# Kernel tuning notes

Measured on AMD Instinct MI355X. Metric: run time of the kernel, lower is better.

The kernel has to match this reference:

```python
import jax, jax.numpy as jnp
import numpy as np

B = 64        # number of graphs
NPG = 4096    # nodes per graph (equal-size segments, batch ids sorted)
H = 256       # hidden_dim
C0, C1 = 256, 64  # num_clusters


def setup_inputs() -> dict:
    key = jax.random.key(0)
    ks = jax.random.split(key, 8)
    N = B * NPG
    x = jax.random.normal(ks[0], (N, H), dtype=jnp.float32)
    edge_index = jax.random.randint(ks[1], (2, N), 0, N, dtype=jnp.int64)  # unused by forward
    batch = jnp.repeat(jnp.arange(B, dtype=jnp.int64), NPG)  # sorted, equal-size segments
    s = 1.0 / np.sqrt(H)
    W0 = jax.random.uniform(ks[2], (H, C0), jnp.float32, -s, s)
    b0 = jax.random.uniform(ks[3], (C0,), jnp.float32, -s, s)
    W1 = jax.random.uniform(ks[4], (H, C1), jnp.float32, -s, s)
    b1 = jax.random.uniform(ks[5], (C1,), jnp.float32, -s, s)
    sf = 1.0 / np.sqrt(C1 * H)
    Wf = jax.random.uniform(ks[6], (C1 * H, H), jnp.float32, -sf, sf)
    bf = jax.random.uniform(ks[7], (H,), jnp.float32, -sf, sf)
    return {"x": x, "edge_index": edge_index, "batch": batch,
            "W0": W0, "b0": b0, "W1": W1, "b1": b1, "Wf": Wf, "bf": bf}


def reference(x, edge_index, batch, W0, b0, W1, b1, Wf, bf):
    # Level 0: softmax cluster assignment + per-graph segmented matmul A^T @ F.
    # batch ids are sorted with equal-size segments, so the per-graph Python
    # loop of the original collapses to a reshape + batched einsum.
    A0 = jax.nn.softmax(x @ W0 + b0, axis=-1)                      # [N, C0]
    f0 = jnp.einsum('bnc,bnh->bch',
                    A0.reshape(B, NPG, C0),
                    x.reshape(B, NPG, H)).reshape(B * C0, H)        # [B*C0, H]
    # Level 1: same pattern on pooled cluster features (C0 'nodes' per graph).
    A1 = jax.nn.softmax(f0 @ W1 + b1, axis=-1)                     # [B*C0, C1]
    f1 = jnp.einsum('bnc,bnh->bch',
                    A1.reshape(B, C0, C1),
                    f0.reshape(B, C0, H)).reshape(B, C1 * H)        # [B, C1*H]
    # Final pool: Linear -> ReLU (Dropout is identity in eval mode).
    return jax.nn.relu(f1 @ Wf + bf)                               # [B, H]
```

## Files before the change

### kernel.cpp

```cpp
#include <hip/hip_runtime.h>
#include <stdint.h>

#define NG   64
#define NPG  4096
#define HD   256
#define NC0  256
#define NC1  64
#define KSPLIT 2

typedef __attribute__((ext_vector_type(8))) short bfx8;
typedef __attribute__((ext_vector_type(4))) float fx4;

__device__ __forceinline__ unsigned short f2bf(float f) {
  union { float f; unsigned int u; } v; v.f = f;
  return (unsigned short)((v.u + 0x7FFFu + ((v.u >> 16) & 1u)) >> 16);
}
__device__ __forceinline__ unsigned int pack2(float a, float b) {
  return (unsigned int)f2bf(a) | ((unsigned int)f2bf(b) << 16);
}

#define ASYNC_COPY16(gptr, lptr) \
  __builtin_amdgcn_global_load_lds((const __attribute__((address_space(1))) unsigned int*)(gptr), \
                                   (__attribute__((address_space(3))) unsigned int*)(lptr), 16, 0, 0)

__global__ __launch_bounds__(256) void k_w0f(const float* __restrict__ W0,
                                             unsigned short* __restrict__ W0F) {
  int gid = blockIdx.x * 256 + threadIdx.x;
  int l15 = gid & 15;
  int q   = (gid >> 4) & 3;
  int ks  = (gid >> 6) & 1;
  int kc  = (gid >> 7) & 3;
  int cblk = gid >> 9;
  int c = cblk * 16 + l15;
  int kb = kc * 64 + ks * 32 + q * 8;
  unsigned int u[4];
  #pragma unroll
  for (int j = 0; j < 8; j += 2)
    u[j >> 1] = pack2(W0[(size_t)(kb + j) * 256 + c], W0[(size_t)(kb + j + 1) * 256 + c]);
  *(float4*)(W0F + (size_t)gid * 8) = *(float4*)u;
}

__global__ __launch_bounds__(512, 4) void k_assign0(
    const float* __restrict__ x, const unsigned short* __restrict__ W0F,
    const float* __restrict__ b0, unsigned short* __restrict__ A0T,
    unsigned short* __restrict__ xT, int g0) {
  __shared__ unsigned short lds_u[18432];
  __shared__ float red[512];

  int gl = blockIdx.x >> 5, nt = blockIdx.x & 31;
  int tid = threadIdx.x;
  int wave = tid >> 6, lane = tid & 63;
  int wm = wave >> 2, wn = wave & 3;
  int l15 = lane & 15, q = lane >> 4;

  fx4 acc[4][4];
  #pragma unroll
  for (int i = 0; i < 4; ++i)
    #pragma unroll
    for (int j = 0; j < 4; ++j) acc[i][j] = fx4{0.f, 0.f, 0.f, 0.f};

  const float* xbase = x + ((size_t)(g0 + gl) * NPG + (size_t)nt * 128) * HD;
  int snode = tid >> 2;
  int sseg  = (tid & 3) * 16;
  int sg0   = (tid & 3) * 2;
  int ssw   = (snode ^ (snode >> 4)) & 7;

  bfx8 bvc[4], bvn[4];
  #pragma unroll
  for (int ni = 0; ni < 4; ++ni)
    bvc[ni] = *(const bfx8*)(W0F + ((size_t)(((wn * 4 + ni) * 8 + 0) * 64 + lane)) * 8);

  {
    const float4* src = (const float4*)(xbase + (size_t)snode * HD + sseg);
    float4 v0 = src[0], v1 = src[1], v2 = src[2], v3 = src[3];
    float4 pv[2]; unsigned int* pu = (unsigned int*)pv;
    pu[0] = pack2(v0.x, v0.y); pu[1] = pack2(v0.z, v0.w);
    pu[2] = pack2(v1.x, v1.y); pu[3] = pack2(v1.z, v1.w);
    pu[4] = pack2(v2.x, v2.y); pu[5] = pack2(v2.z, v2.w);
    pu[6] = pack2(v3.x, v3.y); pu[7] = pack2(v3.z, v3.w);
    unsigned short* drow = &lds_u[snode << 6];
    *(float4*)(drow + (((sg0    ) ^ ssw) << 3)) = pv[0];
    *(float4*)(drow + (((sg0 + 1) ^ ssw) << 3)) = pv[1];
  }
  __syncthreads();

  #pragma unroll
  for (int kc = 0; kc < 4; ++kc) {
    const unsigned short* xb = &lds_u[(kc & 1) * 8192];
    float4 v0, v1, v2, v3;
    if (kc < 3) {
      const float4* src = (const float4*)(xbase + (size_t)snode * HD + (kc + 1) * 64 + sseg);
      v0 = src[0]; v1 = src[1]; v2 = src[2]; v3 = src[3];
    }
    #pragma unroll
    for (int ks = 0; ks < 2; ++ks) {
      int g8 = kc * 2 + ks;
      if (g8 < 7) {
        #pragma unroll
        for (int ni = 0; ni < 4; ++ni)
          bvn[ni] = *(const bfx8*)(W0F + ((size_t)(((wn * 4 + ni) * 8 + g8 + 1) * 64 + lane)) * 8);
      }
      bfx8 af[4];
      #pragma unroll
      for (int mi = 0; mi < 4; ++mi) {
        int row = wm * 64 + mi * 16 + l15;
        int slot = (ks * 4 + q) ^ ((row ^ (row >> 4)) & 7);
        af[mi] = *(const bfx8*)&xb[(row << 6) + (slot << 3)];
      }
      #pragma unroll
      for (int ni = 0; ni < 4; ++ni)
        #pragma unroll
        for (int mi = 0; mi < 4; ++mi)
          acc[mi][ni] = __builtin_amdgcn_mfma_f32_16x16x32_bf16(af[mi], bvc[ni], acc[mi][ni], 0, 0, 0);
      if (g8 < 7) {
        #pragma unroll
        for (int ni = 0; ni < 4; ++ni) bvc[ni] = bvn[ni];
      }
    }
    #pragma unroll
    for (int p2 = 0; p2 < 2; ++p2) {
      int hl = p2 * 32 + wave * 4 + (lane >> 4);
      int g = hl >> 3, off = hl & 7;
      int nb = (lane & 15) * 8;
      unsigned int u[4];
      #pragma unroll
      for (int j = 0; j < 8; j += 2) {
        int n0 = nb + j, n1 = n0 + 1;
        unsigned short a = xb[(n0 << 6) + ((g ^ ((n0 ^ (n0 >> 4)) & 7)) << 3) + off];
        unsigned short b = xb[(n1 << 6) + ((g ^ ((n1 ^ (n1 >> 4)) & 7)) << 3) + off];
        u[j >> 1] = (unsigned int)a | ((unsigned int)b << 16);
      }
      *(float4*)(xT + ((size_t)gl * HD + kc * 64 + hl) * NPG + (size_t)nt * 128 + nb) = *(float4*)u;
    }
    if (kc < 3) {
      float4 pv[2]; unsigned int* pu = (unsigned int*)pv;
      pu[0] = pack2(v0.x, v0.y); pu[1] = pack2(v0.z, v0.w);
      pu[2] = pack2(v1.x, v1.y); pu[3] = pack2(v1.z, v1.w);
      pu[4] = pack2(v2.x, v2.y); pu[5] = pack2(v2.z, v2.w);
      pu[6] = pack2(v3.x, v3.y); pu[7] = pack2(v3.z, v3.w);
      unsigned short* drow = &lds_u[(((kc & 1) ^ 1) * 8192) + (snode << 6)];
      *(float4*)(drow + (((sg0    ) ^ ssw) << 3)) = pv[0];
      *(float4*)(drow + (((sg0 + 1) ^ ssw) << 3)) = pv[1];
    }
    __syncthreads();
  }

  float bv4[4];
  #pragma unroll
  for (int ni = 0; ni < 4; ++ni) bv4[ni] = b0[wn * 64 + ni * 16 + l15];
  #pragma unroll
  for (int mi = 0; mi < 4; ++mi)
    #pragma unroll
    for (int ni = 0; ni < 4; ++ni)
      #pragma unroll
      for (int r = 0; r < 4; ++r) acc[mi][ni][r] += bv4[ni];

  float mrow[4][4];
  #pragma unroll
  for (int mi = 0; mi < 4; ++mi)
    #pragma unroll
    for (int r = 0; r < 4; ++r) {
      float m = fmaxf(fmaxf(acc[mi][0][r], acc[mi][1][r]), fmaxf(acc[mi][2][r], acc[mi][3][r]));
      #pragma unroll
      for (int off = 1; off < 16; off <<= 1) m = fmaxf(m, __shfl_xor(m, off));
      mrow[mi][r] = m;
    }
  if (l15 == 0) {
    #pragma unroll
    for (int mi = 0; mi < 4; ++mi)
      #pragma unroll
      for (int r = 0; r < 4; ++r)
        red[(wm * 64 + mi * 16 + q * 4 + r) * 4 + wn] = mrow[mi][r];
  }
  __syncthreads();
  #pragma unroll
  for (int mi = 0; mi < 4; ++mi)
    #pragma unroll
    for (int r = 0; r < 4; ++r) {
      float4 rv = *(const float4*)&red[(wm * 64 + mi * 16 + q * 4 + r) * 4];
      mrow[mi][r] = fmaxf(fmaxf(rv.x, rv.y), fmaxf(rv.z, rv.w));
    }
  __syncthreads();
  float srow[4][4];
  #pragma unroll
  for (int mi = 0; mi < 4; ++mi)
    #pragma unroll
    for (int r = 0; r < 4; ++r) {
      float s = 0.f;
      #pragma unroll
      for (int ni = 0; ni < 4; ++ni) {
        float e = __expf(acc[mi][ni][r] - mrow[mi][r]);
        acc[mi][ni][r] = e; s += e;
      }
      #pragma unroll
      for (int off = 1; off < 16; off <<= 1) s += __shfl_xor(s, off);
      srow[mi][r] = s;
    }
  if (l15 == 0) {
    #pragma unroll
    for (int mi = 0; mi < 4; ++mi)
      #pragma unroll
      for (int r = 0; r < 4; ++r)
        red[(wm * 64 + mi * 16 + q * 4 + r) * 4 + wn] = srow[mi][r];
  }
  __syncthreads();
  #pragma unroll
  for (int mi = 0; mi < 4; ++mi)
    #pragma unroll
    for (int r = 0; r < 4; ++r) {
      float4 rv = *(const float4*)&red[(wm * 64 + mi * 16 + q * 4 + r) * 4];
      float inv = 1.f / (rv.x + rv.y + rv.z + rv.w);
      #pragma unroll
      for (int ni = 0; ni < 4; ++ni) acc[mi][ni][r] *= inv;
    }
  __syncthreads();

  unsigned short* at = lds_u;
  unsigned short* A0Tg = A0T + (size_t)gl * NC0 * NPG + (size_t)nt * 128;
  #pragma unroll
  for (int p = 0; p < 2; ++p) {
    if ((wn >> 1) == p) {
      int cb = (wn & 1) * 64;
      #pragma unroll
      for (int mi = 0; mi < 4; ++mi) {
        int ncol = wm * 64 + mi * 16 + q * 4;
        #pragma unroll
        for (int ni = 0; ni < 4; ++ni) {
          int cl = cb + ni * 16 + l15;
          uint2 w;
          w.x = pack2(acc[mi][ni][0], acc[mi][ni][1]);
          w.y = pack2(acc[mi][ni][2], acc[mi][ni][3]);
          *(uint2*)(at + cl * 144 + ncol) = w;
        }
      }
    }
    __syncthreads();
    #pragma unroll
    for (int rp = 0; rp < 4; ++rp) {
      int row = rp * 32 + wave * 4 + (lane >> 4);
      int nb = (lane & 15) * 8;
      bfx8 vv = *(const bfx8*)(at + row * 144 + nb);
      *(bfx8*)(A0Tg + (size_t)(p * 128 + row) * NPG + nb) = vv;
    }
    __syncthreads();
  }
}

__global__ __launch_bounds__(256, 2) void k_pool0(
    const unsigned short* __restrict__ A0T, const unsigned short* __restrict__ xT,
    float* __restrict__ f0p, int g0) {
  __shared__ unsigned short a_s[128 * 64];
  __shared__ unsigned short b_s[128 * 64];
  int bid = blockIdx.x;
  int kidx = bid & 1;
  int nt = (bid >> 1) & 1;
  int mt = (bid >> 2) & 1;
  int gl = bid >> 3;

  int tid = threadIdx.x;
  int wave = tid >> 6, lane = tid & 63;
  int wm = wave >> 1, wnn = wave & 1;
  int l15 = lane & 15, q = lane >> 4;

  const int KPER = NPG / KSPLIT;
  const unsigned short* abase = A0T + ((size_t)gl * NC0 + (size_t)mt * 128) * NPG + (size_t)kidx * KPER;
  const unsigned short* bbase = xT  + ((size_t)gl * HD  + (size_t)nt * 128) * NPG + (size_t)kidx * KPER;

  fx4 acc[4][4];
  #pragma unroll
  for (int i = 0; i < 4; ++i)
    #pragma unroll
    for (int j = 0; j < 4; ++j) acc[i][j] = fx4{0.f, 0.f, 0.f, 0.f};

  int srow = lane >> 3;
  int sg   = (lane & 7) ^ srow;
  size_t soff = (size_t)srow * NPG + (size_t)sg * 8;

  for (int k0 = 0; k0 < KPER; k0 += 64) {
    #pragma unroll
    for (int i = 0; i < 4; ++i) {
      int r0 = wave * 32 + i * 8;
      ASYNC_COPY16(abase + (size_t)r0 * NPG + k0 + soff, &a_s[r0 * 64]);
      ASYNC_COPY16(bbase + (size_t)r0 * NPG + k0 + soff, &b_s[r0 * 64]);
    }
    __syncthreads();
    #pragma unroll
    for (int ks = 0; ks < 2; ++ks) {
      int gx = ((ks * 4 + q) ^ (l15 & 7)) << 3;
      bfx8 af[4], bf[4];
      #pragma unroll
      for (int mi = 0; mi < 4; ++mi)
        af[mi] = *(const bfx8*)&a_s[(wm * 64 + mi * 16 + l15) * 64 + gx];
      #pragma unroll
      for (int ni = 0; ni < 4; ++ni)
        bf[ni] = *(const bfx8*)&b_s[(wnn * 64 + ni * 16 + l15) * 64 + gx];
      #pragma unroll
      for (int ni = 0; ni < 4; ++ni)
        #pragma unroll
        for (int mi = 0; mi < 4; ++mi)
          acc[mi][ni] = __builtin_amdgcn_mfma_f32_16x16x32_bf16(af[mi], bf[ni], acc[mi][ni], 0, 0, 0);
    }
    __syncthreads();
  }

  float* dst = f0p + (size_t)kidx * NG * NC0 * HD
             + ((size_t)(g0 + gl) * NC0 + (size_t)mt * 128) * HD + (size_t)nt * 128;
  #pragma unroll
  for (int mi = 0; mi < 4; ++mi)
    #pragma unroll
    for (int ni = 0; ni < 4; ++ni) {
      int c = wm * 64 + mi * 16 + q * 4;
      int h = wnn * 64 + ni * 16 + l15;
      #pragma unroll
      for (int r = 0; r < 4; ++r)
        dst[(size_t)(c + r) * HD + h] = acc[mi][ni][r];
    }
}

__global__ __launch_bounds__(256) void k_f0sum(float* __restrict__ f0) {
  size_t i = ((size_t)blockIdx.x * 256 + threadIdx.x) * 4;
  float4 a = *(const float4*)(f0 + i);
  float4 b = *(const float4*)(f0 + (size_t)NG * NC0 * HD + i);
  a.x += b.x; a.y += b.y; a.z += b.z; a.w += b.w;
  *(float4*)(f0 + i) = a;
}

__global__ __launch_bounds__(256) void k_assign1(
    const float* __restrict__ f0, const float* __restrict__ W1,
    const float* __restrict__ b1, float* __restrict__ A1) {
  __shared__ float w1s[256 * 64];
  int tid = threadIdx.x;
  #pragma unroll
  for (int i = 0; i < 16; ++i) {
    int off = i * 1024 + tid * 4;
    *(float4*)(w1s + off) = *(const float4*)(W1 + off);
  }
  __syncthreads();
  int lane = tid & 63;
  int rbase = blockIdx.x * 32 + (tid >> 6) * 8;
  float bias = b1[lane];
  for (int rr = 0; rr < 8; ++rr) {
    int row = rbase + rr;
    const float* fr = f0 + (size_t)row * 256;
    float acc = bias;
    for (int k = 0; k < 256; k += 4) {
      float4 fv = *(const float4*)(fr + k);
      acc += fv.x * w1s[(k    ) * 64 + lane];
      acc += fv.y * w1s[(k + 1) * 64 + lane];
      acc += fv.z * w1s[(k + 2) * 64 + lane];
      acc += fv.w * w1s[(k + 3) * 64 + lane];
    }
    float m = acc;
    #pragma unroll
    for (int off = 1; off < 64; off <<= 1) m = fmaxf(m, __shfl_xor(m, off));
    float e = __expf(acc - m);
    float s = e;
    #pragma unroll
    for (int off = 1; off < 64; off <<= 1) s += __shfl_xor(s, off);
    A1[(size_t)row * 64 + lane] = e / s;
  }
}

__global__ __launch_bounds__(256) void k_pool1(
    const float* __restrict__ A1, const float* __restrict__ f0, float* __restrict__ f1) {
  int b = blockIdx.x >> 2, cg = blockIdx.x & 3;
  int h = threadIdx.x;
  const float* a1p = A1 + (size_t)b * NC0 * NC1 + cg * 16;
  const float* f0p = f0 + (size_t)b * NC0 * HD + h;
  float acc[16];
  #pragma unroll
  for (int j = 0; j < 16; ++j) acc[j] = 0.f;
  for (int c0 = 0; c0 < 256; ++c0) {
    float fv = f0p[(size_t)c0 * 256];
    #pragma unroll
    for (int j = 0; j < 16; ++j) acc[j] += a1p[c0 * 64 + j] * fv;
  }
  float* d = f1 + (size_t)b * 16384 + (size_t)(cg * 16) * 256 + h;
  #pragma unroll
  for (int j = 0; j < 16; ++j) d[(size_t)j * 256] = acc[j];
}

__global__ __launch_bounds__(512) void k_final_partial(
    const float* __restrict__ f1, const float* __restrict__ Wf, float* __restrict__ ot) {
  __shared__ float f1s[64 * 256];
  int ht = blockIdx.x & 3;
  int ks = blockIdx.x >> 2;
  int tid = threadIdx.x;
  {
    int b = tid >> 3, c0 = (tid & 7) * 4;
    const float* s = f1 + (size_t)b * 16384 + (size_t)ks * 256 + c0;
    float* d = f1s + b * 256 + c0;
    #pragma unroll
    for (int i = 0; i < 8; ++i) *(float4*)(d + i * 32) = *(const float4*)(s + i * 32);
  }
  __syncthreads();
  int h = ht * 64 + (tid & 63);
  int b0 = (tid >> 6) * 8;
  const float* wp = Wf + (size_t)ks * 256 * 256 + h;
  float acc[8];
  #pragma unroll
  for (int j = 0; j < 8; ++j) acc[j] = 0.f;
  for (int k = 0; k < 256; k += 4) {
    float w0 = wp[(size_t)(k    ) * 256];
    float w1 = wp[(size_t)(k + 1) * 256];
    float w2 = wp[(size_t)(k + 2) * 256];
    float w3 = wp[(size_t)(k + 3) * 256];
    #pragma unroll
    for (int j = 0; j < 8; ++j) {
      float4 fv = *(const float4*)(f1s + (b0 + j) * 256 + k);
      acc[j] += fv.x * w0 + fv.y * w1 + fv.z * w2 + fv.w * w3;
    }
  }
  #pragma unroll
  for (int j = 0; j < 8; ++j) atomicAdd(&ot[(b0 + j) * 256 + h], acc[j]);
}

__global__ __launch_bounds__(256) void k_final_out(
    const float* __restrict__ ot, const float* __restrict__ bfv, float* __restrict__ out) {
  int i = blockIdx.x * 256 + threadIdx.x;
  float v = ot[i] + bfv[i & 255];
  out[i] = v > 0.f ? v : 0.f;
}

extern "C" void kernel_launch(void* const* d_in, const int* in_sizes, int n_in,
                              void* d_out, int out_size, void* d_ws, size_t ws_size,
                              hipStream_t stream) {
  const float* x   = (const float*)d_in[0];
  const float* W0  = (const float*)d_in[3];
  const float* b0  = (const float*)d_in[4];
  const float* W1  = (const float*)d_in[5];
  const float* b1  = (const float*)d_in[6];
  const float* Wf  = (const float*)d_in[7];
  const float* bfv = (const float*)d_in[8];
  float* out = (float*)d_out;
  char* ws = (char*)d_ws;

  float* f0p = (float*)ws;
  float* f0  = f0p;
  float* ot  = (float*)(ws + ((size_t)32 << 20));
  unsigned short* W0F = (unsigned short*)(ws + ((size_t)32 << 20) + 65536);
  size_t chunk_off = ((size_t)32 << 20) + 65536 + 131072;
  size_t per_graph = (size_t)4 * HD * NPG;
  size_t avail = ws_size > chunk_off ? ws_size - chunk_off : 0;
  int G = (int)(avail / per_graph);
  if (G > 64) G = 64;
  if (G < 1) G = 1;
  unsigned short* xT  = (unsigned short*)(ws + chunk_off);
  unsigned short* A0T = xT + (size_t)G * HD * NPG;
  float* f1 = (float*)xT;
  float* A1 = (float*)A0T;

  hipMemsetAsync(ot, 0, 65536, stream);
  k_w0f<<<32, 256, 0, stream>>>(W0, W0F);

  for (int g0 = 0; g0 < NG; g0 += G) {
    int gc = (NG - g0 < G) ? (NG - g0) : G;
    k_assign0<<<gc * 32, 512, 0, stream>>>(x, W0F, b0, A0T, xT, g0);
    k_pool0<<<gc * 4 * KSPLIT, 256, 0, stream>>>(A0T, xT, f0p, g0);
  }
  k_f0sum<<<4096, 256, 0, stream>>>(f0);
  k_assign1<<<512, 256, 0, stream>>>(f0, W1, b1, A1);
  k_pool1<<<256, 256, 0, stream>>>(A1, f0, f1);
  k_final_partial<<<256, 512, 0, stream>>>(f1, Wf, ot);
  k_final_out<<<64, 256, 0, stream>>>(ot, bfv, out);
}
```

Before: 735.2 us.

## Remove pool0 K-split, double-buffer pool0 loads, use padded LDS in assign0

k_pool0 drops the two-way K split and the separate k_f0sum reduction kernel. Each 512-thread block now covers the full K range with double-buffered async global-to-LDS copies, so the next tile loads while MFMAs run on the current one. k_assign0 swaps the XOR-swizzled LDS layout for a padded row stride, gets simpler transpose and store paths for xT and A0T, and lowers its launch-bounds occupancy hint. The cost is half as many pool0 blocks (256 blocks on a many-CU GPU), which may underfill the device, plus possible bank conflicts from the padded layout.

```diff
diff --git a/kernel.cpp b/kernel.cpp
--- a/kernel.cpp
+++ b/kernel.cpp
@@ -6,7 +6,6 @@
 #define HD   256
 #define NC0  256
 #define NC1  64
-#define KSPLIT 2
 
 typedef __attribute__((ext_vector_type(8))) short bfx8;
 typedef __attribute__((ext_vector_type(4))) float fx4;
@@ -40,12 +39,14 @@
   *(float4*)(W0F + (size_t)gid * 8) = *(float4*)u;
 }
 
-__global__ __launch_bounds__(512, 4) void k_assign0(
+#define XSP 72
+__global__ __launch_bounds__(512, 2) void k_assign0(
     const float* __restrict__ x, const unsigned short* __restrict__ W0F,
     const float* __restrict__ b0, unsigned short* __restrict__ A0T,
     unsigned short* __restrict__ xT, int g0) {
-  __shared__ unsigned short lds_u[18432];
-  __shared__ float red[512];
+  __shared__ unsigned short xs[2][128 * XSP];
+  __shared__ float red[128 * 4];
+  unsigned short* at = (unsigned short*)xs;
 
   int gl = blockIdx.x >> 5, nt = blockIdx.x & 31;
   int tid = threadIdx.x;
@@ -60,10 +61,7 @@
     for (int j = 0; j < 4; ++j) acc[i][j] = fx4{0.f, 0.f, 0.f, 0.f};
 
   const float* xbase = x + ((size_t)(g0 + gl) * NPG + (size_t)nt * 128) * HD;
-  int snode = tid >> 2;
-  int sseg  = (tid & 3) * 16;
-  int sg0   = (tid & 3) * 2;
-  int ssw   = (snode ^ (snode >> 4)) & 7;
+  int snode = tid >> 2, sseg = (tid & 3) * 16;
 
   bfx8 bvc[4], bvn[4];
   #pragma unroll
@@ -78,15 +76,13 @@
     pu[2] = pack2(v1.x, v1.y); pu[3] = pack2(v1.z, v1.w);
     pu[4] = pack2(v2.x, v2.y); pu[5] = pack2(v2.z, v2.w);
     pu[6] = pack2(v3.x, v3.y); pu[7] = pack2(v3.z, v3.w);
-    unsigned short* drow = &lds_u[snode << 6];
-    *(float4*)(drow + (((sg0    ) ^ ssw) << 3)) = pv[0];
-    *(float4*)(drow + (((sg0 + 1) ^ ssw) << 3)) = pv[1];
-  }
-  __syncthreads();
-
-  #pragma unroll
+    float4* d = (float4*)&xs[0][snode * XSP + sseg];
+    d[0] = pv[0]; d[1] = pv[1];
+  }
+  __syncthreads();
+
   for (int kc = 0; kc < 4; ++kc) {
-    const unsigned short* xb = &lds_u[(kc & 1) * 8192];
+    int buf = kc & 1;
     float4 v0, v1, v2, v3;
     if (kc < 3) {
       const float4* src = (const float4*)(xbase + (size_t)snode * HD + (kc + 1) * 64 + sseg);
@@ -100,13 +96,11 @@
         for (int ni = 0; ni < 4; ++ni)
           bvn[ni] = *(const bfx8*)(W0F + ((size_t)(((wn * 4 + ni) * 8 + g8 + 1) * 64 + lane)) * 8);
       }
+      int kk = ks * 32 + q * 8;
       bfx8 af[4];
       #pragma unroll
-      for (int mi = 0; mi < 4; ++mi) {
-        int row = wm * 64 + mi * 16 + l15;
-        int slot = (ks * 4 + q) ^ ((row ^ (row >> 4)) & 7);
-        af[mi] = *(const bfx8*)&xb[(row << 6) + (slot << 3)];
-      }
+      for (int mi = 0; mi < 4; ++mi)
+        af[mi] = *(const bfx8*)&xs[buf][(wm * 64 + mi * 16 + l15) * XSP + kk];
       #pragma unroll
       for (int ni = 0; ni < 4; ++ni)
         #pragma unroll
@@ -117,20 +111,19 @@
         for (int ni = 0; ni < 4; ++ni) bvc[ni] = bvn[ni];
       }
     }
-    #pragma unroll
-    for (int p2 = 0; p2 < 2; ++p2) {
-      int hl = p2 * 32 + wave * 4 + (lane >> 4);
-      int g = hl >> 3, off = hl & 7;
-      int nb = (lane & 15) * 8;
-      unsigned int u[4];
-      #pragma unroll
-      for (int j = 0; j < 8; j += 2) {
-        int n0 = nb + j, n1 = n0 + 1;
-        unsigned short a = xb[(n0 << 6) + ((g ^ ((n0 ^ (n0 >> 4)) & 7)) << 3) + off];
-        unsigned short b = xb[(n1 << 6) + ((g ^ ((n1 ^ (n1 >> 4)) & 7)) << 3) + off];
-        u[j >> 1] = (unsigned int)a | ((unsigned int)b << 16);
-      }
-      *(float4*)(xT + ((size_t)gl * HD + kc * 64 + hl) * NPG + (size_t)nt * 128 + nb) = *(float4*)u;
+    {
+      int hl = tid >> 3;
+      int seg = (tid & 7) * 16;
+      unsigned int u[8];
+      #pragma unroll
+      for (int i = 0; i < 16; i += 2) {
+        unsigned short a = xs[buf][(seg + i) * XSP + hl];
+        unsigned short b = xs[buf][(seg + i + 1) * XSP + hl];
+        u[i >> 1] = (unsigned int)a | ((unsigned int)b << 16);
+      }
+      float4* dst = (float4*)(xT + ((size_t)gl * HD + kc * 64 + hl) * NPG + (size_t)nt * 128 + seg);
+      dst[0] = *(float4*)&u[0];
+      dst[1] = *(float4*)&u[4];
     }
     if (kc < 3) {
       float4 pv[2]; unsigned int* pu = (unsigned int*)pv;
@@ -138,9 +131,8 @@
       pu[2] = pack2(v1.x, v1.y); pu[3] = pack2(v1.z, v1.w);
       pu[4] = pack2(v2.x, v2.y); pu[5] = pack2(v2.z, v2.w);
       pu[6] = pack2(v3.x, v3.y); pu[7] = pack2(v3.z, v3.w);
-      unsigned short* drow = &lds_u[(((kc & 1) ^ 1) * 8192) + (snode << 6)];
-      *(float4*)(drow + (((sg0    ) ^ ssw) << 3)) = pv[0];
-      *(float4*)(drow + (((sg0 + 1) ^ ssw) << 3)) = pv[1];
+      float4* d = (float4*)&xs[buf ^ 1][snode * XSP + sseg];
+      d[0] = pv[0]; d[1] = pv[1];
     }
     __syncthreads();
   }
@@ -215,7 +207,6 @@
     }
   __syncthreads();
 
-  unsigned short* at = lds_u;
   unsigned short* A0Tg = A0T + (size_t)gl * NC0 * NPG + (size_t)nt * 128;
   #pragma unroll
   for (int p = 0; p < 2; ++p) {
@@ -230,72 +221,81 @@
           uint2 w;
           w.x = pack2(acc[mi][ni][0], acc[mi][ni][1]);
           w.y = pack2(acc[mi][ni][2], acc[mi][ni][3]);
-          *(uint2*)(at + cl * 144 + ncol) = w;
+          *(uint2*)(at + cl * 136 + ncol) = w;
         }
       }
     }
     __syncthreads();
-    #pragma unroll
-    for (int rp = 0; rp < 4; ++rp) {
-      int row = rp * 32 + wave * 4 + (lane >> 4);
-      int nb = (lane & 15) * 8;
-      bfx8 vv = *(const bfx8*)(at + row * 144 + nb);
-      *(bfx8*)(A0Tg + (size_t)(p * 128 + row) * NPG + nb) = vv;
+    {
+      int row = tid >> 2, seg = (tid & 3) * 32;
+      const float4* s4 = (const float4*)(at + row * 136 + seg);
+      float4 a = s4[0], b = s4[1], c = s4[2], d = s4[3];
+      float4* d4 = (float4*)(A0Tg + (size_t)(p * 128 + row) * NPG + seg);
+      d4[0] = a; d4[1] = b; d4[2] = c; d4[3] = d;
     }
     __syncthreads();
   }
 }
 
-__global__ __launch_bounds__(256, 2) void k_pool0(
+__global__ __launch_bounds__(512, 2) void k_pool0(
     const unsigned short* __restrict__ A0T, const unsigned short* __restrict__ xT,
-    float* __restrict__ f0p, int g0) {
-  __shared__ unsigned short a_s[128 * 64];
-  __shared__ unsigned short b_s[128 * 64];
+    float* __restrict__ f0, int g0) {
+  __shared__ unsigned short a_s[2][128 * 64];
+  __shared__ unsigned short b_s[2][128 * 64];
   int bid = blockIdx.x;
-  int kidx = bid & 1;
-  int nt = (bid >> 1) & 1;
-  int mt = (bid >> 2) & 1;
-  int gl = bid >> 3;
+  int nt = bid & 1;
+  int mt = (bid >> 1) & 1;
+  int gl = bid >> 2;
 
   int tid = threadIdx.x;
   int wave = tid >> 6, lane = tid & 63;
-  int wm = wave >> 1, wnn = wave & 1;
+  int wm = wave >> 2, wn = wave & 3;
   int l15 = lane & 15, q = lane >> 4;
 
-  const int KPER = NPG / KSPLIT;
-  const unsigned short* abase = A0T + ((size_t)gl * NC0 + (size_t)mt * 128) * NPG + (size_t)kidx * KPER;
-  const unsigned short* bbase = xT  + ((size_t)gl * HD  + (size_t)nt * 128) * NPG + (size_t)kidx * KPER;
-
-  fx4 acc[4][4];
+  const unsigned short* abase = A0T + ((size_t)gl * NC0 + (size_t)mt * 128) * NPG;
+  const unsigned short* bbase = xT  + ((size_t)gl * HD  + (size_t)nt * 128) * NPG;
+
+  fx4 acc[4][2];
   #pragma unroll
   for (int i = 0; i < 4; ++i)
     #pragma unroll
-    for (int j = 0; j < 4; ++j) acc[i][j] = fx4{0.f, 0.f, 0.f, 0.f};
+    for (int j = 0; j < 2; ++j) acc[i][j] = fx4{0.f, 0.f, 0.f, 0.f};
 
   int srow = lane >> 3;
   int sg   = (lane & 7) ^ srow;
   size_t soff = (size_t)srow * NPG + (size_t)sg * 8;
 
-  for (int k0 = 0; k0 < KPER; k0 += 64) {
-    #pragma unroll
-    for (int i = 0; i < 4; ++i) {
-      int r0 = wave * 32 + i * 8;
-      ASYNC_COPY16(abase + (size_t)r0 * NPG + k0 + soff, &a_s[r0 * 64]);
-      ASYNC_COPY16(bbase + (size_t)r0 * NPG + k0 + soff, &b_s[r0 * 64]);
-    }
-    __syncthreads();
+  #pragma unroll
+  for (int i = 0; i < 2; ++i) {
+    int r0 = wave * 16 + i * 8;
+    ASYNC_COPY16(abase + (size_t)r0 * NPG + soff, &a_s[0][r0 * 64]);
+    ASYNC_COPY16(bbase + (size_t)r0 * NPG + soff, &b_s[0][r0 * 64]);
+  }
+  __syncthreads();
+
+  for (int t = 0; t < NPG / 64; ++t) {
+    int buf = t & 1;
+    if (t < NPG / 64 - 1) {
+      int k0 = (t + 1) * 64;
+      #pragma unroll
+      for (int i = 0; i < 2; ++i) {
+        int r0 = wave * 16 + i * 8;
+        ASYNC_COPY16(abase + (size_t)r0 * NPG + k0 + soff, &a_s[buf ^ 1][r0 * 64]);
+        ASYNC_COPY16(bbase + (size_t)r0 * NPG + k0 + soff, &b_s[buf ^ 1][r0 * 64]);
+      }
+    }
     #pragma unroll
     for (int ks = 0; ks < 2; ++ks) {
       int gx = ((ks * 4 + q) ^ (l15 & 7)) << 3;
-      bfx8 af[4], bf[4];
+      bfx8 af[4], bf[2];
       #pragma unroll
       for (int mi = 0; mi < 4; ++mi)
-        af[mi] = *(const bfx8*)&a_s[(wm * 64 + mi * 16 + l15) * 64 + gx];
-      #pragma unroll
-      for (int ni = 0; ni < 4; ++ni)
-        bf[ni] = *(const bfx8*)&b_s[(wnn * 64 + ni * 16 + l15) * 64 + gx];
-      #pragma unroll
-      for (int ni = 0; ni < 4; ++ni)
+        af[mi] = *(const bfx8*)&a_s[buf][(wm * 64 + mi * 16 + l15) * 64 + gx];
+      #pragma unroll
+      for (int ni = 0; ni < 2; ++ni)
+        bf[ni] = *(const bfx8*)&b_s[buf][(wn * 32 + ni * 16 + l15) * 64 + gx];
+      #pragma unroll
+      for (int ni = 0; ni < 2; ++ni)
         #pragma unroll
         for (int mi = 0; mi < 4; ++mi)
           acc[mi][ni] = __builtin_amdgcn_mfma_f32_16x16x32_bf16(af[mi], bf[ni], acc[mi][ni], 0, 0, 0);
@@ -303,26 +303,17 @@
     __syncthreads();
   }
 
-  float* dst = f0p + (size_t)kidx * NG * NC0 * HD
-             + ((size_t)(g0 + gl) * NC0 + (size_t)mt * 128) * HD + (size_t)nt * 128;
-  #pragma unroll
-  for (int mi = 0; mi < 4; ++mi)
-    #pragma unroll
-    for (int ni = 0; ni < 4; ++ni) {
+  float* dst = f0 + ((size_t)(g0 + gl) * NC0 + (size_t)mt * 128) * HD + (size_t)nt * 128;
+  #pragma unroll
+  for (int mi = 0; mi < 4; ++mi)
+    #pragma unroll
+    for (int ni = 0; ni < 2; ++ni) {
       int c = wm * 64 + mi * 16 + q * 4;
-      int h = wnn * 64 + ni * 16 + l15;
+      int h = wn * 32 + ni * 16 + l15;
       #pragma unroll
       for (int r = 0; r < 4; ++r)
         dst[(size_t)(c + r) * HD + h] = acc[mi][ni][r];
     }
-}
-
-__global__ __launch_bounds__(256) void k_f0sum(float* __restrict__ f0) {
-  size_t i = ((size_t)blockIdx.x * 256 + threadIdx.x) * 4;
-  float4 a = *(const float4*)(f0 + i);
-  float4 b = *(const float4*)(f0 + (size_t)NG * NC0 * HD + i);
-  a.x += b.x; a.y += b.y; a.z += b.z; a.w += b.w;
-  *(float4*)(f0 + i) = a;
 }
 
 __global__ __launch_bounds__(256) void k_assign1(
@@ -435,8 +426,7 @@
   float* out = (float*)d_out;
   char* ws = (char*)d_ws;
 
-  float* f0p = (float*)ws;
-  float* f0  = f0p;
+  float* f0  = (float*)ws;
   float* ot  = (float*)(ws + ((size_t)32 << 20));
   unsigned short* W0F = (unsigned short*)(ws + ((size_t)32 << 20) + 65536);
   size_t chunk_off = ((size_t)32 << 20) + 65536 + 131072;
@@ -456,9 +446,8 @@
   for (int g0 = 0; g0 < NG; g0 += G) {
     int gc = (NG - g0 < G) ? (NG - g0) : G;
     k_assign0<<<gc * 32, 512, 0, stream>>>(x, W0F, b0, A0T, xT, g0);
-    k_pool0<<<gc * 4 * KSPLIT, 256, 0, stream>>>(A0T, xT, f0p, g0);
-  }
-  k_f0sum<<<4096, 256, 0, stream>>>(f0);
+    k_pool0<<<gc * 4, 512, 0, stream>>>(A0T, xT, f0, g0);
+  }
   k_assign1<<<512, 256, 0, stream>>>(f0, W1, b1, A1);
   k_pool1<<<256, 256, 0, stream>>>(A1, f0, f1);
   k_final_partial<<<256, 512, 0, stream>>>(f1, Wf, ot);
```

Result: faster. 690.7 us (-6.1%).
